# Performance work log

Measured on AMD Instinct MI355X. Metric: run time of the kernel, lower is better.

Reference implementation:

```python
import jax, jax.numpy as jnp
import numpy as np
import math

B, T, D = 2, 2048, 2048
H, HKV = 32, 8
DH = D // H          # 64
G = H // HKV         # 4 query heads per kv head
ROPE_BASE = 10000.0


def _rope_cos_sin(t, dh):
    inv_freq = 1.0 / (ROPE_BASE ** (jnp.arange(0, dh, 2, dtype=jnp.float32) / dh))
    pos = jnp.arange(t, dtype=jnp.float32)
    freqs = pos[:, None] * inv_freq[None, :]          # [T, Dh/2]
    emb = jnp.concatenate([freqs, freqs], axis=-1)    # [T, Dh]
    return jnp.cos(emb), jnp.sin(emb)


def _rotate_half(y):
    y1, y2 = jnp.split(y, 2, axis=-1)
    return jnp.concatenate([-y2, y1], axis=-1)


def _apply_rope(x, cos, sin):  # x: [..., T, Dh]; cos/sin: [T, Dh]
    return x * cos + _rotate_half(x) * sin


def setup_inputs() -> dict:
    key = jax.random.key(0)
    k = jax.random.split(key, 5)
    x = jax.random.normal(k[0], (B, T, D), dtype=jnp.float32)
    Wq = jax.random.normal(k[1], (D, D), dtype=jnp.float32) * 0.02
    Wk = jax.random.normal(k[2], (D, HKV * DH), dtype=jnp.float32) * 0.02
    Wv = jax.random.normal(k[3], (D, HKV * DH), dtype=jnp.float32) * 0.02
    Wo = jax.random.normal(k[4], (D, D), dtype=jnp.float32) * 0.02
    causal = jnp.tril(jnp.ones((T, T), dtype=bool))
    attn_mask = jnp.where(causal, 0.0, -1e9).astype(jnp.float32)[None, None]  # [1,1,T,T]
    return {"x": x, "Wq": Wq, "Wk": Wk, "Wv": Wv, "Wo": Wo, "attn_mask": attn_mask}


def reference(x, Wq, Wk, Wv, Wo, attn_mask):
    Bx, Tx, Dx = x.shape
    # projections (Linear, no bias)
    q = (x @ Wq).reshape(Bx, Tx, H, DH).transpose(0, 2, 1, 3)      # [B,H,T,Dh]
    kk = (x @ Wk).reshape(Bx, Tx, HKV, DH).transpose(0, 2, 1, 3)   # [B,Hkv,T,Dh]
    vv = (x @ Wv).reshape(Bx, Tx, HKV, DH).transpose(0, 2, 1, 3)   # [B,Hkv,T,Dh]
    # RoPE on q and k (offset=0, no kv cache)
    cos, sin = _rope_cos_sin(Tx, DH)
    q = _apply_rope(q, cos, sin)
    kk = _apply_rope(kk, cos, sin)
    # GQA: group query heads so head h uses kv head h // G (matches repeat_interleave)
    qg = q.reshape(Bx, HKV, G, Tx, DH)
    att = jnp.einsum('bkgtd,bksd->bkgts', qg, kk) / math.sqrt(DH)
    att = att + attn_mask[:, :, None]                              # broadcast over groups
    p = jax.nn.softmax(att, axis=-1)
    ctx = jnp.einsum('bkgts,bksd->bkgtd', p, vv)                   # [B,Hkv,G,T,Dh]
    ctx = ctx.reshape(Bx, H, Tx, DH).transpose(0, 2, 1, 3).reshape(Bx, Tx, Dx)
    return ctx @ Wo
```

## Files before the change

### kernel.cpp

```cpp
#include <hip/hip_runtime.h>
#include <hip/hip_bf16.h>


typedef __bf16 bf16_t;
typedef __bf16 bf16x4 __attribute__((ext_vector_type(4)));
typedef __bf16 bf16x8 __attribute__((ext_vector_type(8)));
typedef float f32x4 __attribute__((ext_vector_type(4)));

#define B_ 2
#define T_ 2048
#define D_ 2048
#define H_ 32
#define HKV_ 8
#define DH_ 64

__device__ __forceinline__ float fast_exp2(float x) { return __builtin_amdgcn_exp2f(x); }

__device__ __forceinline__ void gld_lds16(const bf16_t* g, bf16_t* l) {
  __builtin_amdgcn_global_load_lds((const __attribute__((address_space(1))) unsigned int*)g,
                                   (__attribute__((address_space(3))) unsigned int*)l, 16, 0, 0);
}

__global__ __launch_bounds__(256) void cast_f32_bf16(const float* __restrict__ in,
                                                     bf16_t* __restrict__ out, int n) {
  int i = (blockIdx.x * 256 + threadIdx.x) * 8;
  if (i < n) {
    f32x4 a = *(const f32x4*)&in[i];
    f32x4 b = *(const f32x4*)&in[i + 4];
    bf16x8 o;
    o[0] = (bf16_t)a[0]; o[1] = (bf16_t)a[1]; o[2] = (bf16_t)a[2]; o[3] = (bf16_t)a[3];
    o[4] = (bf16_t)b[0]; o[5] = (bf16_t)b[1]; o[6] = (bf16_t)b[2]; o[7] = (bf16_t)b[3];
    *(bf16x8*)&out[i] = o;
  }
}

__global__ __launch_bounds__(256) void transpose_w(const float* __restrict__ W,
                                                   bf16_t* __restrict__ Wt, int K, int N) {
  __shared__ float tile[64][65];
  int n0 = blockIdx.x * 64, k0 = blockIdx.y * 64;
  int tid = threadIdx.x;
  for (int i = tid; i < 4096; i += 256) {
    int r = i >> 6, c = i & 63;
    tile[r][c] = W[(size_t)(k0 + r) * N + n0 + c];
  }
  __syncthreads();
  for (int i = tid; i < 4096; i += 256) {
    int r = i >> 6, c = i & 63;
    Wt[(size_t)(n0 + r) * K + k0 + c] = (bf16_t)tile[c][r];
  }
}

__global__ __launch_bounds__(256) void transpose_wqkv(const float* __restrict__ Wq,
                                                      const float* __restrict__ Wk,
                                                      const float* __restrict__ Wv,
                                                      bf16_t* __restrict__ Wt) {
  __shared__ float tile[64][65];
  int n0 = blockIdx.x * 64, k0 = blockIdx.y * 64;
  const float* W;
  int srcN, col;
  if (n0 < 2048) { W = Wq; srcN = 2048; col = n0; }
  else if (n0 < 2560) { W = Wk; srcN = 512; col = n0 - 2048; }
  else { W = Wv; srcN = 512; col = n0 - 2560; }
  int tid = threadIdx.x;
  for (int i = tid; i < 4096; i += 256) {
    int r = i >> 6, c = i & 63;
    tile[r][c] = W[(size_t)(k0 + r) * srcN + col + c];
  }
  __syncthreads();
  for (int i = tid; i < 4096; i += 256) {
    int r = i >> 6, c = i & 63;
    Wt[(size_t)(n0 + r) * 2048 + k0 + c] = (bf16_t)tile[c][r];
  }
}

template <typename OutT>
__global__ __launch_bounds__(256) void gemm_bt(const bf16_t* __restrict__ A,
                                               const bf16_t* __restrict__ Bt,
                                               OutT* __restrict__ C, int M, int N, int K) {
  __shared__ __align__(16) bf16_t As[2 * 128 * 32];
  __shared__ __align__(16) bf16_t Bs[2 * 128 * 32];
  int tid = threadIdx.x;
  int lane = tid & 63;
  int wave = tid >> 6;
  int l15 = lane & 15;
  int quad = lane >> 4;
  int m0 = blockIdx.y * 128;
  int n0 = blockIdx.x * 128;
  int wrow = (wave >> 1) * 64;
  int wcol = (wave & 1) * 64;

  f32x4 acc[4][4] = {};

  for (int kc = 0; kc < K; kc += 64) {
#pragma unroll
    for (int kk = 0; kk < 2; ++kk) {
#pragma unroll
      for (int c = 0; c < 2; ++c) {
        int linear = c * 256 + tid;
        int r = linear >> 2, seg = linear & 3;
        gld_lds16(&A[(size_t)(m0 + r) * K + kc + kk * 32 + seg * 8],
                  &As[kk * 4096 + (size_t)(c * 256 + wave * 64) * 8]);
        gld_lds16(&Bt[(size_t)(n0 + r) * K + kc + kk * 32 + seg * 8],
                  &Bs[kk * 4096 + (size_t)(c * 256 + wave * 64) * 8]);
      }
    }
    __syncthreads();
#pragma unroll
    for (int kk = 0; kk < 2; ++kk) {
      bf16x8 af[4], bfr[4];
#pragma unroll
      for (int mi = 0; mi < 4; ++mi)
        af[mi] = *(const bf16x8*)&As[kk * 4096 + (wrow + mi * 16 + l15) * 32 + quad * 8];
#pragma unroll
      for (int ni = 0; ni < 4; ++ni)
        bfr[ni] = *(const bf16x8*)&Bs[kk * 4096 + (wcol + ni * 16 + l15) * 32 + quad * 8];
#pragma unroll
      for (int mi = 0; mi < 4; ++mi)
#pragma unroll
        for (int ni = 0; ni < 4; ++ni)
          acc[mi][ni] = __builtin_amdgcn_mfma_f32_16x16x32_bf16(af[mi], bfr[ni], acc[mi][ni], 0, 0, 0);
    }
    __syncthreads();
  }
#pragma unroll
  for (int mi = 0; mi < 4; ++mi) {
#pragma unroll
    for (int ni = 0; ni < 4; ++ni) {
#pragma unroll
      for (int r = 0; r < 4; ++r) {
        int m = m0 + wrow + mi * 16 + quad * 4 + r;
        int n = n0 + wcol + ni * 16 + l15;
        C[(size_t)m * N + n] = (OutT)acc[mi][ni][r];
      }
    }
  }
}

__global__ __launch_bounds__(256) void rope_qk(const bf16_t* __restrict__ qkv,
                                               bf16_t* __restrict__ qr,
                                               bf16_t* __restrict__ kr) {
  int t = blockIdx.x, b = blockIdx.y;
  int tid = threadIdx.x;
  const bf16_t* row = qkv + (size_t)(b * T_ + t) * 3072;
  const float LN1E4_over32 = 9.210340371976184f / 32.0f;
  const float QSC = 1.44269504088896f * 0.125f;
  int ksw = (t & 7) << 3;
  for (int i = tid; i < 1024 + 256; i += 256) {
    bool isq = i < 1024;
    int ii = isq ? i : i - 1024;
    int hh = ii >> 5, j = ii & 31;
    int base = isq ? 0 : 2048;
    float inv = __expf(-(float)j * LN1E4_over32);
    float fr = (float)t * inv;
    float sn, cs;
    sincosf(fr, &sn, &cs);
    float x1 = (float)row[base + hh * 64 + j];
    float x2 = (float)row[base + hh * 64 + j + 32];
    float o1 = x1 * cs - x2 * sn;
    float o2 = x2 * cs + x1 * sn;
    if (isq) {
      size_t o = ((size_t)(b * H_ + hh) * T_ + t) * DH_;
      qr[o + j] = (bf16_t)(o1 * QSC);
      qr[o + j + 32] = (bf16_t)(o2 * QSC);
    } else {
      size_t o = ((size_t)(b * HKV_ + hh) * T_ + t) * DH_;
      kr[o + (j ^ ksw)] = (bf16_t)o1;
      kr[o + ((j + 32) ^ ksw)] = (bf16_t)o2;
    }
  }
}

__global__ __launch_bounds__(256) void transpose_v(const bf16_t* __restrict__ qkv,
                                                   bf16_t* __restrict__ vtr) {
  __shared__ __align__(16) bf16_t tile[64][72];
  int t0 = blockIdx.x * 64;
  int hk = blockIdx.y;
  int b = blockIdx.z;
  int tid = threadIdx.x;
  for (int i = tid; i < 512; i += 256) {
    int r = i >> 3, s = i & 7;
    *(bf16x8*)&tile[r][s * 8] =
        *(const bf16x8*)&qkv[(size_t)(b * T_ + t0 + r) * 3072 + 2560 + hk * 64 + s * 8];
  }
  __syncthreads();
  for (int i = tid; i < 4096; i += 256) {
    int dd = i >> 6, tt = i & 63;
    int src = (tt & 32) | ((tt & 4) << 2) | ((tt & 24) >> 1) | (tt & 3);
    int dst = tt ^ ((dd & 7) << 3);
    vtr[((size_t)(b * HKV_ + hk) * DH_ + dd) * T_ + t0 + dst] = tile[src][dd];
  }
}

#define DO_HALF(QF, O, LACC, DOMASK, KS, VT)                                              \
  {                                                                                       \
    f32x4 s_[4] = {};                                                                     \
    _Pragma("unroll") for (int mt = 0; mt < 4; ++mt) {                                    \
      bf16x8 ak0 = *(const bf16x8*)&KS[(mt * 16 + l15) * 64 + ((quad * 8) ^ swz)];        \
      bf16x8 ak1 = *(const bf16x8*)&KS[(mt * 16 + l15) * 64 + ((32 + quad * 8) ^ swz)];   \
      s_[mt] = __builtin_amdgcn_mfma_f32_16x16x32_bf16(ak0, QF[0], s_[mt], 0, 0, 0);      \
      s_[mt] = __builtin_amdgcn_mfma_f32_16x16x32_bf16(ak1, QF[1], s_[mt], 0, 0, 0);      \
    }                                                                                     \
    if (DOMASK) {                                                                         \
      _Pragma("unroll") for (int mt = 0; mt < 4; ++mt)                                    \
          _Pragma("unroll") for (int r = 0; r < 4; ++r) if (mt * 16 + quad * 4 + r >      \
                                                            wave * 16 + l15)              \
              s_[mt][r] = -1e30f;                                                         \
    }                                                                                     \
    _Pragma("unroll") for (int k0 = 0; k0 < 2; ++k0) {                                    \
      bf16x8 pa;                                                                          \
      _Pragma("unroll") for (int hh = 0; hh < 2; ++hh)                                    \
          _Pragma("unroll") for (int r = 0; r < 4; ++r) {                                 \
        float p = fast_exp2(s_[2 * k0 + hh][r]);                                          \
        LACC += p;                                                                        \
        pa[hh * 4 + r] = (bf16_t)p;                                                       \
      }                                                                                   \
      _Pragma("unroll") for (int dn = 0; dn < 4; ++dn) {                                  \
        bf16x8 bv =                                                                       \
            *(const bf16x8*)&VT[(dn * 16 + l15) * 64 + ((k0 * 32 + quad * 8) ^ swz)];     \
        O[dn] = __builtin_amdgcn_mfma_f32_16x16x32_bf16(pa, bv, O[dn], 0, 0, 0);          \
      }                                                                                   \
    }                                                                                     \
  }

__global__ __launch_bounds__(256) void flash_attn(const bf16_t* __restrict__ qr,
                                                  const bf16_t* __restrict__ kr,
                                                  const bf16_t* __restrict__ vtr,
                                                  bf16_t* __restrict__ ctxb) {
  __shared__ __align__(16) bf16_t Ks[2][64 * 64];
  __shared__ __align__(16) bf16_t Vt[2][64 * 64];
  int tid = threadIdx.x;
  int lane = tid & 63;
  int wave = tid >> 6;
  int l15 = lane & 15, quad = lane >> 4;
  int swz = (l15 & 7) * 8;
  int pair = blockIdx.x, h = blockIdx.y, b = blockIdx.z;
  int qtA = pair, qtB = 31 - pair;
  int nkvA = qtA + 1, nkvB = qtB + 1;
  int kvh = h >> 2;

  const bf16_t* qbA = qr + ((size_t)(b * H_ + h) * T_ + qtA * 64 + wave * 16) * DH_;
  const bf16_t* qbB = qr + ((size_t)(b * H_ + h) * T_ + qtB * 64 + wave * 16) * DH_;
  const bf16_t* kbase = kr + (size_t)(b * HKV_ + kvh) * T_ * DH_;
  const bf16_t* vbase = vtr + (size_t)(b * HKV_ + kvh) * DH_ * T_;

  bf16x8 qA[2], qB[2];
#pragma unroll
  for (int k0 = 0; k0 < 2; ++k0) {
    qA[k0] = *(const bf16x8*)&qbA[l15 * 64 + k0 * 32 + quad * 8];
    qB[k0] = *(const bf16x8*)&qbB[l15 * 64 + k0 * 32 + quad * 8];
  }

  f32x4 oA[4] = {}, oB[4] = {};
  float lA = 0.f, lB = 0.f;

  auto stage = [&](int kv, int bf) {
#pragma unroll
    for (int c = 0; c < 2; ++c) {
      int idx = c * 256 + tid;
      bf16_t* dst = &Ks[bf][(c * 256 + wave * 64) * 8];
      gld_lds16(&kbase[(size_t)kv * 4096 + idx * 8], dst);
      bf16_t* dstv = &Vt[bf][(c * 256 + wave * 64) * 8];
      gld_lds16(&vbase[(size_t)(idx >> 3) * T_ + kv * 64 + (idx & 7) * 8], dstv);
    }
  };
  stage(0, 0);

  for (int kv = 0; kv < nkvB; ++kv) {
    const bf16_t* ks = Ks[kv & 1];
    const bf16_t* vt = Vt[kv & 1];
    __syncthreads();
    if (kv + 1 < nkvB) stage(kv + 1, (kv + 1) & 1);

    DO_HALF(qB, oB, lB, kv == qtB, ks, vt);
    if (kv < nkvA) DO_HALF(qA, oA, lA, kv == qtA, ks, vt);
  }

  lA += __shfl_xor(lA, 16, 64);
  lA += __shfl_xor(lA, 32, 64);
  lB += __shfl_xor(lB, 16, 64);
  lB += __shfl_xor(lB, 32, 64);
  float invA = 1.0f / lA, invB = 1.0f / lB;
#pragma unroll
  for (int r = 0; r < 4; ++r) {
    float iAr = __shfl(invA, quad * 4 + r, 64);
    float iBr = __shfl(invB, quad * 4 + r, 64);
    int tA = qtA * 64 + wave * 16 + quad * 4 + r;
    int tB = qtB * 64 + wave * 16 + quad * 4 + r;
#pragma unroll
    for (int dn = 0; dn < 4; ++dn) {
      ctxb[(size_t)(b * T_ + tA) * D_ + h * 64 + dn * 16 + l15] = (bf16_t)(oA[dn][r] * iAr);
      ctxb[(size_t)(b * T_ + tB) * D_ + h * 64 + dn * 16 + l15] = (bf16_t)(oB[dn][r] * iBr);
    }
  }
}

extern "C" void kernel_launch(void* const* d_in, const int* in_sizes, int n_in,
                              void* d_out, int out_size, void* d_ws, size_t ws_size,
                              hipStream_t stream) {
  const float* x = (const float*)d_in[0];
  const float* Wq = (const float*)d_in[1];
  const float* Wk = (const float*)d_in[2];
  const float* Wv = (const float*)d_in[3];
  const float* Wo = (const float*)d_in[4];
  float* out = (float*)d_out;

  char* ws = (char*)d_ws;
  size_t off = 0;
  bf16_t* xb = (bf16_t*)(ws + off); off += (size_t)B_ * T_ * D_ * 2;
  bf16_t* wqkvb = (bf16_t*)(ws + off); off += (size_t)3072 * 2048 * 2;
  bf16_t* wob = (bf16_t*)(ws + off); off += (size_t)2048 * 2048 * 2;
  bf16_t* qkv = (bf16_t*)(ws + off); off += (size_t)4096 * 3072 * 2;
  bf16_t* qr = (bf16_t*)(ws + off); off += (size_t)B_ * H_ * T_ * DH_ * 2;
  bf16_t* kr = (bf16_t*)(ws + off); off += (size_t)B_ * HKV_ * T_ * DH_ * 2;
  bf16_t* vtr = (bf16_t*)(ws + off); off += (size_t)B_ * HKV_ * T_ * DH_ * 2;
  bf16_t* ctxb = (bf16_t*)(ws + off); off += (size_t)B_ * T_ * D_ * 2;

  int nx = B_ * T_ * D_;
  cast_f32_bf16<<<nx / 8 / 256, 256, 0, stream>>>(x, xb, nx);
  transpose_wqkv<<<dim3(3072 / 64, 2048 / 64), 256, 0, stream>>>(Wq, Wk, Wv, wqkvb);
  transpose_w<<<dim3(2048 / 64, 2048 / 64), 256, 0, stream>>>(Wo, wob, 2048, 2048);

  gemm_bt<bf16_t><<<dim3(3072 / 128, 4096 / 128), 256, 0, stream>>>(xb, wqkvb, qkv, 4096, 3072, 2048);

  rope_qk<<<dim3(T_, B_), 256, 0, stream>>>(qkv, qr, kr);
  transpose_v<<<dim3(T_ / 64, HKV_, B_), 256, 0, stream>>>(qkv, vtr);

  flash_attn<<<dim3(16, H_, B_), 256, 0, stream>>>(qr, kr, vtr, ctxb);

  gemm_bt<float><<<dim3(2048 / 128, 4096 / 128), 256, 0, stream>>>(ctxb, wob, out, 4096, 2048, 2048);
}
```

Before: 324.8 us.

## Assign each wave 32 rows of one query tile instead of splitting across both

Flash attention previously gave every wave 16 rows of both paired query tiles (the early tile A and the late tile B). Now waves 0-1 each take 32 rows of tile A and waves 2-3 each take 32 rows of tile B. Each K and V fragment read from LDS now feeds two MFMA row groups, halving LDS reads per MFMA and adding instruction-level parallelism. The cost is load imbalance: the tile-A waves sit idle once their shorter kv range ends, while the tile-B waves run every iteration. This lengthens the per-block critical path and keeps more accumulator registers live.

```diff
diff --git a/kernel.cpp b/kernel.cpp
--- a/kernel.cpp
+++ b/kernel.cpp
@@ -191,37 +191,6 @@
   }
 }
 
-#define DO_HALF(QF, O, LACC, DOMASK, KS, VT)                                              \
-  {                                                                                       \
-    f32x4 s_[4] = {};                                                                     \
-    _Pragma("unroll") for (int mt = 0; mt < 4; ++mt) {                                    \
-      bf16x8 ak0 = *(const bf16x8*)&KS[(mt * 16 + l15) * 64 + ((quad * 8) ^ swz)];        \
-      bf16x8 ak1 = *(const bf16x8*)&KS[(mt * 16 + l15) * 64 + ((32 + quad * 8) ^ swz)];   \
-      s_[mt] = __builtin_amdgcn_mfma_f32_16x16x32_bf16(ak0, QF[0], s_[mt], 0, 0, 0);      \
-      s_[mt] = __builtin_amdgcn_mfma_f32_16x16x32_bf16(ak1, QF[1], s_[mt], 0, 0, 0);      \
-    }                                                                                     \
-    if (DOMASK) {                                                                         \
-      _Pragma("unroll") for (int mt = 0; mt < 4; ++mt)                                    \
-          _Pragma("unroll") for (int r = 0; r < 4; ++r) if (mt * 16 + quad * 4 + r >      \
-                                                            wave * 16 + l15)              \
-              s_[mt][r] = -1e30f;                                                         \
-    }                                                                                     \
-    _Pragma("unroll") for (int k0 = 0; k0 < 2; ++k0) {                                    \
-      bf16x8 pa;                                                                          \
-      _Pragma("unroll") for (int hh = 0; hh < 2; ++hh)                                    \
-          _Pragma("unroll") for (int r = 0; r < 4; ++r) {                                 \
-        float p = fast_exp2(s_[2 * k0 + hh][r]);                                          \
-        LACC += p;                                                                        \
-        pa[hh * 4 + r] = (bf16_t)p;                                                       \
-      }                                                                                   \
-      _Pragma("unroll") for (int dn = 0; dn < 4; ++dn) {                                  \
-        bf16x8 bv =                                                                       \
-            *(const bf16x8*)&VT[(dn * 16 + l15) * 64 + ((k0 * 32 + quad * 8) ^ swz)];     \
-        O[dn] = __builtin_amdgcn_mfma_f32_16x16x32_bf16(pa, bv, O[dn], 0, 0, 0);          \
-      }                                                                                   \
-    }                                                                                     \
-  }
-
 __global__ __launch_bounds__(256) void flash_attn(const bf16_t* __restrict__ qr,
                                                   const bf16_t* __restrict__ kr,
                                                   const bf16_t* __restrict__ vtr,
@@ -235,23 +204,26 @@
   int swz = (l15 & 7) * 8;
   int pair = blockIdx.x, h = blockIdx.y, b = blockIdx.z;
   int qtA = pair, qtB = 31 - pair;
-  int nkvA = qtA + 1, nkvB = qtB + 1;
+  int nkvB = qtB + 1;
   int kvh = h >> 2;
 
-  const bf16_t* qbA = qr + ((size_t)(b * H_ + h) * T_ + qtA * 64 + wave * 16) * DH_;
-  const bf16_t* qbB = qr + ((size_t)(b * H_ + h) * T_ + qtB * 64 + wave * 16) * DH_;
+  int myQt = (wave < 2) ? qtA : qtB;
+  int nkv = myQt + 1;
+  int wrow = (wave & 1) * 32;
+
+  const bf16_t* qb = qr + ((size_t)(b * H_ + h) * T_ + myQt * 64 + wrow) * DH_;
   const bf16_t* kbase = kr + (size_t)(b * HKV_ + kvh) * T_ * DH_;
   const bf16_t* vbase = vtr + (size_t)(b * HKV_ + kvh) * DH_ * T_;
 
-  bf16x8 qA[2], qB[2];
-#pragma unroll
-  for (int k0 = 0; k0 < 2; ++k0) {
-    qA[k0] = *(const bf16x8*)&qbA[l15 * 64 + k0 * 32 + quad * 8];
-    qB[k0] = *(const bf16x8*)&qbB[l15 * 64 + k0 * 32 + quad * 8];
-  }
-
-  f32x4 oA[4] = {}, oB[4] = {};
-  float lA = 0.f, lB = 0.f;
+  bf16x8 q[2][2];
+#pragma unroll
+  for (int rg = 0; rg < 2; ++rg)
+#pragma unroll
+    for (int k0 = 0; k0 < 2; ++k0)
+      q[rg][k0] = *(const bf16x8*)&qb[(rg * 16 + l15) * 64 + k0 * 32 + quad * 8];
+
+  f32x4 o[2][4] = {};
+  float l0 = 0.f, l1 = 0.f;
 
   auto stage = [&](int kv, int bf) {
 #pragma unroll
@@ -271,25 +243,69 @@
     __syncthreads();
     if (kv + 1 < nkvB) stage(kv + 1, (kv + 1) & 1);
 
-    DO_HALF(qB, oB, lB, kv == qtB, ks, vt);
-    if (kv < nkvA) DO_HALF(qA, oA, lA, kv == qtA, ks, vt);
-  }
-
-  lA += __shfl_xor(lA, 16, 64);
-  lA += __shfl_xor(lA, 32, 64);
-  lB += __shfl_xor(lB, 16, 64);
-  lB += __shfl_xor(lB, 32, 64);
-  float invA = 1.0f / lA, invB = 1.0f / lB;
+    if (kv < nkv) {
+      f32x4 s[2][4] = {};
+#pragma unroll
+      for (int mt = 0; mt < 4; ++mt) {
+        bf16x8 ak0 = *(const bf16x8*)&ks[(mt * 16 + l15) * 64 + ((quad * 8) ^ swz)];
+        bf16x8 ak1 = *(const bf16x8*)&ks[(mt * 16 + l15) * 64 + ((32 + quad * 8) ^ swz)];
+        s[0][mt] = __builtin_amdgcn_mfma_f32_16x16x32_bf16(ak0, q[0][0], s[0][mt], 0, 0, 0);
+        s[0][mt] = __builtin_amdgcn_mfma_f32_16x16x32_bf16(ak1, q[0][1], s[0][mt], 0, 0, 0);
+        s[1][mt] = __builtin_amdgcn_mfma_f32_16x16x32_bf16(ak0, q[1][0], s[1][mt], 0, 0, 0);
+        s[1][mt] = __builtin_amdgcn_mfma_f32_16x16x32_bf16(ak1, q[1][1], s[1][mt], 0, 0, 0);
+      }
+
+      if (kv == myQt) {
+#pragma unroll
+        for (int rg = 0; rg < 2; ++rg)
+#pragma unroll
+          for (int mt = 0; mt < 4; ++mt)
+#pragma unroll
+            for (int r = 0; r < 4; ++r)
+              if (mt * 16 + quad * 4 + r > wrow + rg * 16 + l15) s[rg][mt][r] = -1e30f;
+      }
+
+      bf16x8 pa[2][2];
+#pragma unroll
+      for (int rg = 0; rg < 2; ++rg)
+#pragma unroll
+        for (int k0 = 0; k0 < 2; ++k0)
+#pragma unroll
+          for (int hh = 0; hh < 2; ++hh)
+#pragma unroll
+            for (int r = 0; r < 4; ++r) {
+              float p = fast_exp2(s[rg][2 * k0 + hh][r]);
+              if (rg == 0) l0 += p; else l1 += p;
+              pa[rg][k0][hh * 4 + r] = (bf16_t)p;
+            }
+
+#pragma unroll
+      for (int k0 = 0; k0 < 2; ++k0) {
+#pragma unroll
+        for (int dn = 0; dn < 4; ++dn) {
+          bf16x8 bv = *(const bf16x8*)&vt[(dn * 16 + l15) * 64 + ((k0 * 32 + quad * 8) ^ swz)];
+          o[0][dn] = __builtin_amdgcn_mfma_f32_16x16x32_bf16(pa[0][k0], bv, o[0][dn], 0, 0, 0);
+          o[1][dn] = __builtin_amdgcn_mfma_f32_16x16x32_bf16(pa[1][k0], bv, o[1][dn], 0, 0, 0);
+        }
+      }
+    }
+  }
+
+  l0 += __shfl_xor(l0, 16, 64);
+  l0 += __shfl_xor(l0, 32, 64);
+  l1 += __shfl_xor(l1, 16, 64);
+  l1 += __shfl_xor(l1, 32, 64);
+  float inv0 = 1.0f / l0, inv1 = 1.0f / l1;
 #pragma unroll
   for (int r = 0; r < 4; ++r) {
-    float iAr = __shfl(invA, quad * 4 + r, 64);
-    float iBr = __shfl(invB, quad * 4 + r, 64);
-    int tA = qtA * 64 + wave * 16 + quad * 4 + r;
-    int tB = qtB * 64 + wave * 16 + quad * 4 + r;
+    float i0 = __shfl(inv0, quad * 4 + r, 64);
+    float i1 = __shfl(inv1, quad * 4 + r, 64);
+    int t0 = myQt * 64 + wrow + quad * 4 + r;
+    int t1 = myQt * 64 + wrow + 16 + quad * 4 + r;
 #pragma unroll
     for (int dn = 0; dn < 4; ++dn) {
-      ctxb[(size_t)(b * T_ + tA) * D_ + h * 64 + dn * 16 + l15] = (bf16_t)(oA[dn][r] * iAr);
-      ctxb[(size_t)(b * T_ + tB) * D_ + h * 64 + dn * 16 + l15] = (bf16_t)(oB[dn][r] * iBr);
+      ctxb[(size_t)(b * T_ + t0) * D_ + h * 64 + dn * 16 + l15] = (bf16_t)(o[0][dn][r] * i0);
+      ctxb[(size_t)(b * T_ + t1) * D_ + h * 64 + dn * 16 + l15] = (bf16_t)(o[1][dn][r] * i1);
     }
   }
 }
```

Result: slower. 357.1 us (+9.9%).
